# Kernel optimization log

Hardware: AMD Instinct MI355X
Metric: run time of the kernel (lower is better)

## Reference

```python
import jax, jax.numpy as jnp
import numpy as np

B, L, D = 4, 1024, 1024
H = 16
DH = D // H  # 64
CACHE_LEN = 1024


def setup_inputs() -> dict:
    key = jax.random.key(0)
    ks = jax.random.split(key, 12)
    s = 1.0 / np.sqrt(D)
    return {
        "query": jax.random.normal(ks[0], (B, L, D), jnp.float32),
        "key": jax.random.normal(ks[1], (B, L, D), jnp.float32),
        "value": jax.random.normal(ks[2], (B, L, D), jnp.float32),
        "cache": jax.random.normal(ks[3], (B, H, CACHE_LEN, 2 * DH), jnp.float32),
        "Wq": jax.random.normal(ks[4], (D, D), jnp.float32) * s,
        "bq": jnp.zeros((D,), jnp.float32),
        "Wk": jax.random.normal(ks[5], (D, D), jnp.float32) * s,
        "bk": jnp.zeros((D,), jnp.float32),
        "Wv": jax.random.normal(ks[6], (D, D), jnp.float32) * s,
        "bv": jnp.zeros((D,), jnp.float32),
        "Wo": jax.random.normal(ks[7], (D, D), jnp.float32) * s,
        "bo": jnp.zeros((D,), jnp.float32),
    }


def _split_heads(x):
    # (B, L, D) -> (B, H, L, DH)
    b, l, _ = x.shape
    return x.reshape(b, l, H, DH).transpose(0, 2, 1, 3)


def reference(query, key, value, cache, Wq, bq, Wk, bk, Wv, bv, Wo, bo):
    q = _split_heads(query @ Wq.T + bq)   # (B,H,Lq,DH)
    k = _split_heads(key @ Wk.T + bk)     # (B,H,Lk,DH)
    v = _split_heads(value @ Wv.T + bv)   # (B,H,Lk,DH)

    # KV-cache concat along sequence dim
    key_cache, value_cache = jnp.split(cache, 2, axis=-1)
    k = jnp.concatenate([key_cache, k], axis=2)   # (B,H,Lc+Lk,DH)
    v = jnp.concatenate([value_cache, v], axis=2)
    new_cache = jnp.concatenate([k, v], axis=-1)  # (B,H,Lc+Lk,2*DH)

    scores = jnp.einsum("bhqd,bhkd->bhqk", q, k) / jnp.sqrt(jnp.float32(DH))
    attn = jax.nn.softmax(scores, axis=-1)        # unmasked path (mask sentinel empty)
    out = jnp.einsum("bhqk,bhkd->bhqd", attn, v)  # (B,H,Lq,DH)
    out = out.transpose(0, 2, 1, 3).reshape(query.shape[0], -1, H * DH)
    out = out @ Wo.T + bo                         # (B,Lq,D)
    return (out, new_cache)
```

## Files before the change

kernel.cpp:

```cpp
#include <hip/hip_runtime.h>
#include <hip/hip_bf16.h>
#include <stdint.h>

constexpr int Hh = 16, Ll = 1024, Dd = 1024, DHh = 64, CL = 1024, TKV = 2048;
constexpr size_t OUT_ELEMS = 4ull * 1024 * 1024;
constexpr float LOG2E = 1.44269504088896340736f;

typedef __attribute__((ext_vector_type(8))) short short8;
typedef __attribute__((ext_vector_type(4))) float floatx4;

#define MFMA16(a, b, c) __builtin_amdgcn_mfma_f32_16x16x32_bf16(a, b, c, 0, 0, 0)

__device__ __forceinline__ float fexp2(float x) {
#if __has_builtin(__builtin_amdgcn_exp2f)
    return __builtin_amdgcn_exp2f(x);
#else
    float r;
    asm("v_exp_f32 %0, %1" : "=v"(r) : "v"(x));
    return r;
#endif
}

__device__ __forceinline__ short bfs(float x) {
    union { __hip_bfloat16 h; short s; } u;
    u.h = __float2bfloat16(x);
    return u.s;
}

__device__ __forceinline__ short8 cvt8(const float* p) {
    float4 a = *(const float4*)p;
    float4 b = *(const float4*)(p + 4);
    short8 r;
    r[0] = bfs(a.x); r[1] = bfs(a.y); r[2] = bfs(a.z); r[3] = bfs(a.w);
    r[4] = bfs(b.x); r[5] = bfs(b.y); r[6] = bfs(b.z); r[7] = bfs(b.w);
    return r;
}

__device__ __forceinline__ void gload_lds16(const __hip_bfloat16* g, __hip_bfloat16* l) {
    __builtin_amdgcn_global_load_lds((const __attribute__((address_space(1))) void*)g,
                                     (__attribute__((address_space(3))) void*)l, 16, 0, 0);
}

__device__ __forceinline__ int vswz(int d) { return ((d >> 3) ^ d) & 7; }

__global__ __launch_bounds__(256) void prep_kernel(
    const float* __restrict__ cache, const float* __restrict__ Wq,
    const float* __restrict__ Wk, const float* __restrict__ Wv,
    const float* __restrict__ Wo, float* __restrict__ outc,
    __hip_bfloat16* __restrict__ Wb, __hip_bfloat16* __restrict__ kbf,
    __hip_bfloat16* __restrict__ vbf) {
    if (blockIdx.x < 4096) {
        int c = blockIdx.x * 256 + threadIdx.x;
        int bh  = c >> 14;
        int rem = c & 16383;
        int t = rem >> 4, part = rem & 15;
        const float* s = cache + (size_t)c * 8;
        float* d = outc + OUT_ELEMS + (size_t)bh * 262144 + (size_t)rem * 8;
        *(float4*)d       = *(const float4*)s;
        *(float4*)(d + 4) = *(const float4*)(s + 4);
        short8 bv = cvt8(s);
        if (part < 8) {
            *(short8*)&kbf[(size_t)bh * 131072 + (size_t)t * 64 +
                           ((part ^ (t & 7)) << 3)] = bv;
        } else {
            int d0 = (part - 8) * 8;
#pragma unroll
            for (int e = 0; e < 8; e++) {
                int dd = d0 + e;
                ((short*)vbf)[((size_t)(bh * 16 + (t >> 7)) * 64 + dd) * 128 +
                              ((t & 127) ^ (vswz(dd) << 3))] = bv[e];
            }
        }
    } else {
        int c = (blockIdx.x - 4096) * 256 + threadIdx.x;
        int wsel = c >> 17;
        int within = c & 131071;
        const float* src = (wsel == 0) ? Wq : (wsel == 1) ? Wk : (wsel == 2) ? Wv : Wo;
        *(short8*)(Wb + (size_t)c * 8) = cvt8(src + (size_t)within * 8);
    }
}

__global__ __launch_bounds__(256) void gemm_qkv(
    const float* __restrict__ Aq, const float* __restrict__ Ak,
    const float* __restrict__ Av, const __hip_bfloat16* __restrict__ Wb,
    const float* __restrict__ bq, const float* __restrict__ bk,
    const float* __restrict__ bv, __hip_bfloat16* __restrict__ qws,
    float* __restrict__ outc, __hip_bfloat16* __restrict__ kbf,
    __hip_bfloat16* __restrict__ vbf) {
    constexpr int K = 1024, BK = 64;
    __shared__ alignas(16) __hip_bfloat16 As[64 * BK];
    __shared__ alignas(16) __hip_bfloat16 Bs[128 * BK];

    const int mode = blockIdx.z;
    const float* A = (mode == 0) ? Aq : (mode == 1) ? Ak : Av;
    const float* bias = (mode == 0) ? bq : (mode == 1) ? bk : bv;
    const __hip_bfloat16* W = Wb + ((size_t)mode << 20);

    const int tid = threadIdx.x;
    const int w = tid >> 6, lane = tid & 63;
    const int g = lane >> 4, lr = lane & 15;
    const int tm = blockIdx.x * 64, tn = blockIdx.y * 128;
    const int wr = (w >> 1) * 32, wc = (w & 1) * 64;

    floatx4 acc[2][4] = {};

    for (int k0 = 0; k0 < K; k0 += BK) {
        __syncthreads();
#pragma unroll
        for (int it = 0; it < 4; it++) {
            int c0 = it * 256 + w * 64;
            int c = c0 + lane;
            int row = c >> 3, col = (c & 7) * 8;
            gload_lds16(W + (size_t)(tn + row) * K + k0 + col, &Bs[c0 * 8]);
        }
#pragma unroll
        for (int it = 0; it < 2; it++) {
            int c = it * 256 + tid;
            int row = c >> 3, col = (c & 7) * 8;
            *(short8*)&As[c * 8] = cvt8(A + (size_t)(tm + row) * K + k0 + col);
        }
        __syncthreads();
#pragma unroll
        for (int kk = 0; kk < 2; kk++) {
            short8 af[2], bf[4];
#pragma unroll
            for (int i = 0; i < 2; i++)
                af[i] = *(const short8*)&As[(wr + i * 16 + lr) * BK + kk * 32 + g * 8];
#pragma unroll
            for (int j = 0; j < 4; j++)
                bf[j] = *(const short8*)&Bs[(wc + j * 16 + lr) * BK + kk * 32 + g * 8];
#pragma unroll
            for (int i = 0; i < 2; i++)
#pragma unroll
                for (int j = 0; j < 4; j++)
                    acc[i][j] = MFMA16(af[i], bf[j], acc[i][j]);
        }
    }

#pragma unroll
    for (int j = 0; j < 4; j++) {
        int n = tn + wc + j * 16 + lr;
        float bv_ = bias[n];
#pragma unroll
        for (int i = 0; i < 2; i++) {
#pragma unroll
            for (int r = 0; r < 4; r++) {
                int m = tm + wr + i * 16 + g * 4 + r;
                float v = acc[i][j][r] + bv_;
                if (mode == 0) {
                    size_t addr = (size_t)(m >> 10) * ((size_t)Hh * Ll * DHh) +
                                  (size_t)(n >> 6) * ((size_t)Ll * DHh) +
                                  (size_t)(m & 1023) * DHh + (n & 63);
                    qws[addr] = __float2bfloat16(v * (0.125f * LOG2E));
                } else {
                    size_t bh = (size_t)((m >> 10) * Hh + (n >> 6));
                    size_t addr = OUT_ELEMS + (bh * TKV + CL + (m & 1023)) * 128 + (n & 63) +
                                  (mode == 2 ? 64 : 0);
                    outc[addr] = v;
                    int t = CL + (m & 1023);
                    int dd = n & 63;
                    __hip_bfloat16 hv = __float2bfloat16(v);
                    if (mode == 1) {
                        kbf[bh * 131072 + (size_t)t * 64 +
                            (((dd >> 3) ^ (t & 7)) << 3) + (dd & 7)] = hv;
                    } else {
                        vbf[(bh * 16 + (size_t)(t >> 7)) * 8192 + (size_t)dd * 128 +
                            ((t & 127) ^ (vswz(dd) << 3))] = hv;
                    }
                }
            }
        }
    }
}

__global__ __launch_bounds__(256) void gemm_out(
    const __hip_bfloat16* __restrict__ A, const __hip_bfloat16* __restrict__ W,
    const float* __restrict__ bias, float* __restrict__ C) {
    constexpr int K = 1024, BK = 64;
    __shared__ alignas(16) __hip_bfloat16 As[64 * BK];
    __shared__ alignas(16) __hip_bfloat16 Bs[128 * BK];

    const int tid = threadIdx.x;
    const int w = tid >> 6, lane = tid & 63;
    const int g = lane >> 4, lr = lane & 15;
    const int tm = blockIdx.x * 64, tn = blockIdx.y * 128;
    const int wr = (w >> 1) * 32, wc = (w & 1) * 64;

    floatx4 acc[2][4] = {};

    for (int k0 = 0; k0 < K; k0 += BK) {
        __syncthreads();
#pragma unroll
        for (int it = 0; it < 4; it++) {
            int c0 = it * 256 + w * 64;
            int c = c0 + lane;
            int row = c >> 3, col = (c & 7) * 8;
            gload_lds16(W + (size_t)(tn + row) * K + k0 + col, &Bs[c0 * 8]);
        }
#pragma unroll
        for (int it = 0; it < 2; it++) {
            int c0 = it * 256 + w * 64;
            int c = c0 + lane;
            int row = c >> 3, col = (c & 7) * 8;
            gload_lds16(A + (size_t)(tm + row) * K + k0 + col, &As[c0 * 8]);
        }
        __syncthreads();
#pragma unroll
        for (int kk = 0; kk < 2; kk++) {
            short8 af[2], bf[4];
#pragma unroll
            for (int i = 0; i < 2; i++)
                af[i] = *(const short8*)&As[(wr + i * 16 + lr) * BK + kk * 32 + g * 8];
#pragma unroll
            for (int j = 0; j < 4; j++)
                bf[j] = *(const short8*)&Bs[(wc + j * 16 + lr) * BK + kk * 32 + g * 8];
#pragma unroll
            for (int i = 0; i < 2; i++)
#pragma unroll
                for (int j = 0; j < 4; j++)
                    acc[i][j] = MFMA16(af[i], bf[j], acc[i][j]);
        }
    }

#pragma unroll
    for (int j = 0; j < 4; j++) {
        int n = tn + wc + j * 16 + lr;
        float bv = bias[n];
#pragma unroll
        for (int i = 0; i < 2; i++)
#pragma unroll
            for (int r = 0; r < 4; r++) {
                int m = tm + wr + i * 16 + g * 4 + r;
                C[(size_t)m * 1024 + n] = acc[i][j][r] + bv;
            }
    }
}

__global__ __launch_bounds__(512) void attn_kernel(
    const __hip_bfloat16* __restrict__ qws, const __hip_bfloat16* __restrict__ kbf,
    const __hip_bfloat16* __restrict__ vbf, __hip_bfloat16* __restrict__ ows) {
    constexpr int KVB = 128;
    __shared__ alignas(16) __hip_bfloat16 Ks[2][KVB * 64];
    __shared__ alignas(16) __hip_bfloat16 Vt[2][64 * KVB];
    __shared__ alignas(16) __hip_bfloat16 Ps[8][32 * 136];

    const int tid = threadIdx.x;
    const int w = tid >> 6, lane = tid & 63;
    const int g = lane >> 4, lr = lane & 15;
    const int bh = blockIdx.x;
    const int q0 = blockIdx.y * 256 + w * 32;

    const __hip_bfloat16* qbase = qws + (size_t)bh * Ll * DHh;
    const __hip_bfloat16* kb = kbf + (size_t)bh * 131072;
    const __hip_bfloat16* vb = vbf + (size_t)bh * 131072;

    short8 qf[2][2];
#pragma unroll
    for (int i = 0; i < 2; i++)
#pragma unroll
        for (int kk = 0; kk < 2; kk++)
            qf[i][kk] = *(const short8*)
                (qbase + (size_t)(q0 + i * 16 + lr) * DHh + kk * 32 + g * 8);

#define STAGE(b, tl)                                                          \
    {                                                                         \
        const __hip_bfloat16* kt = kb + (size_t)(tl) * 8192;                  \
        const __hip_bfloat16* vt = vb + (size_t)(tl) * 8192;                  \
        _Pragma("unroll")                                                     \
        for (int it = 0; it < 2; it++) {                                      \
            int c0 = it * 512 + w * 64;                                       \
            gload_lds16(kt + (size_t)(c0 + lane) * 8, &Ks[b][c0 * 8]);        \
            gload_lds16(vt + (size_t)(c0 + lane) * 8, &Vt[b][c0 * 8]);        \
        }                                                                     \
    }

    float rm[2][4], rl[2][4];
    floatx4 o[2][4] = {};
#pragma unroll
    for (int i = 0; i < 2; i++)
#pragma unroll
        for (int j = 0; j < 4; j++) { rm[i][j] = -3e38f; rl[i][j] = 0.f; }

    STAGE(0, 0);
    __syncthreads();

    int cur = 0;
    for (int tl = 0; tl < 16; ++tl) {
        if (tl < 15) STAGE(cur ^ 1, tl + 1);

        floatx4 s[2][8] = {};
#pragma unroll
        for (int f = 0; f < 8; f++) {
            int row = f * 16 + lr;
#pragma unroll
            for (int kk = 0; kk < 2; kk++) {
                short8 bfr = *(const short8*)
                    &Ks[cur][row * 64 + (((kk * 4 + g) ^ (row & 7)) << 3)];
                s[0][f] = MFMA16(qf[0][kk], bfr, s[0][f]);
                s[1][f] = MFMA16(qf[1][kk], bfr, s[1][f]);
            }
        }

        bool ok = true;
        float mt[2][4];
#pragma unroll
        for (int i = 0; i < 2; i++)
#pragma unroll
            for (int j = 0; j < 4; j++) {
                float mv = fmaxf(
                    fmaxf(fmaxf(s[i][0][j], s[i][1][j]), fmaxf(s[i][2][j], s[i][3][j])),
                    fmaxf(fmaxf(s[i][4][j], s[i][5][j]), fmaxf(s[i][6][j], s[i][7][j])));
                mv = fmaxf(mv, __shfl_xor(mv, 1));
                mv = fmaxf(mv, __shfl_xor(mv, 2));
                mv = fmaxf(mv, __shfl_xor(mv, 4));
                mv = fmaxf(mv, __shfl_xor(mv, 8));
                mt[i][j] = mv;
                ok = ok && (mv - rm[i][j] <= 8.f);
            }
        if (!__all(ok)) {
#pragma unroll
            for (int i = 0; i < 2; i++)
#pragma unroll
                for (int j = 0; j < 4; j++) {
                    float mn = fmaxf(rm[i][j], mt[i][j]);
                    float corr = fexp2(rm[i][j] - mn);
                    rm[i][j] = mn;
                    rl[i][j] *= corr;
#pragma unroll
                    for (int f2 = 0; f2 < 4; f2++) o[i][f2][j] = o[i][f2][j] * corr;
                }
        }
#pragma unroll
        for (int i = 0; i < 2; i++) {
            float rs[4] = {0.f, 0.f, 0.f, 0.f};
#pragma unroll
            for (int f = 0; f < 8; f++)
#pragma unroll
                for (int j = 0; j < 4; j++) {
                    float p = fexp2(s[i][f][j] - rm[i][j]);
                    s[i][f][j] = p;
                    rs[j] += p;
                }
#pragma unroll
            for (int j = 0; j < 4; j++) {
                rs[j] += __shfl_xor(rs[j], 1);
                rs[j] += __shfl_xor(rs[j], 2);
                rs[j] += __shfl_xor(rs[j], 4);
                rs[j] += __shfl_xor(rs[j], 8);
                rl[i][j] += rs[j];
            }
        }

        __hip_bfloat16* pw = &Ps[w][0];
#pragma unroll
        for (int i = 0; i < 2; i++)
#pragma unroll
            for (int f = 0; f < 8; f++)
#pragma unroll
                for (int j = 0; j < 4; j++)
                    pw[(i * 16 + g * 4 + j) * 136 + f * 16 + lr] =
                        __float2bfloat16(s[i][f][j]);

#pragma unroll
        for (int kk = 0; kk < 4; kk++) {
            short8 pa0 = *(const short8*)&pw[(0 + lr) * 136 + kk * 32 + g * 8];
            short8 pa1 = *(const short8*)&pw[(16 + lr) * 136 + kk * 32 + g * 8];
#pragma unroll
            for (int f2 = 0; f2 < 4; f2++) {
                int d = f2 * 16 + lr;
                short8 vbr = *(const short8*)
                    &Vt[cur][d * KVB + ((kk * 32 + g * 8) ^ (vswz(d) << 3))];
                o[0][f2] = MFMA16(pa0, vbr, o[0][f2]);
                o[1][f2] = MFMA16(pa1, vbr, o[1][f2]);
            }
        }

        __syncthreads();
        cur ^= 1;
    }
#undef STAGE

    const int b = bh >> 4, h = bh & 15;
#pragma unroll
    for (int i = 0; i < 2; i++)
#pragma unroll
        for (int j = 0; j < 4; j++) {
            float inv = 1.0f / rl[i][j];
            int qrow = q0 + i * 16 + g * 4 + j;
            size_t rb = ((size_t)b * Ll + qrow) * Dd + (size_t)h * DHh;
#pragma unroll
            for (int f2 = 0; f2 < 4; f2++)
                ows[rb + f2 * 16 + lr] = __float2bfloat16(o[i][f2][j] * inv);
        }
}

extern "C" void kernel_launch(void* const* d_in, const int* in_sizes, int n_in,
                              void* d_out, int out_size, void* d_ws, size_t ws_size,
                              hipStream_t stream) {
    (void)in_sizes; (void)n_in; (void)out_size; (void)ws_size;
    const float* query = (const float*)d_in[0];
    const float* key   = (const float*)d_in[1];
    const float* value = (const float*)d_in[2];
    const float* cache = (const float*)d_in[3];
    const float* Wq = (const float*)d_in[4];
    const float* bq = (const float*)d_in[5];
    const float* Wk = (const float*)d_in[6];
    const float* bk = (const float*)d_in[7];
    const float* Wv = (const float*)d_in[8];
    const float* bv = (const float*)d_in[9];
    const float* Wo = (const float*)d_in[10];
    const float* bo = (const float*)d_in[11];

    float* out = (float*)d_out;
    __hip_bfloat16* qws = (__hip_bfloat16*)d_ws;
    __hip_bfloat16* aws = qws + OUT_ELEMS;
    __hip_bfloat16* Wb  = aws + OUT_ELEMS;
    __hip_bfloat16* kbf = Wb  + OUT_ELEMS;
    __hip_bfloat16* vbf = kbf + (8ull << 20);

    dim3 bb(256);
    prep_kernel<<<dim3(6144), bb, 0, stream>>>(cache, Wq, Wk, Wv, Wo, out, Wb, kbf, vbf);

    gemm_qkv<<<dim3(64, 8, 3), bb, 0, stream>>>(query, key, value, Wb, bq, bk, bv,
                                                qws, out, kbf, vbf);

    attn_kernel<<<dim3(64, 4), dim3(512), 0, stream>>>(qws, kbf, vbf, aws);

    gemm_out<<<dim3(64, 8), bb, 0, stream>>>(aws, Wb + (3u << 20), bo, out);
}
```

Before: 176.7 us.

## Move KV-cache copy and conversion into QKV GEMM launch as extra z-slice

The cache copy and bf16 conversion into the new_cache output and the K/V attention buffers now run in a fourth z-slice of the QKV GEMM grid. Each of those 512 blocks handles 2048 chunks. The standalone prep kernel is reduced to weight conversion only. This lets the memory-bound cache copy overlap with the compute-bound projection GEMM and shrinks the serial prep launch, but it puts bandwidth-heavy blocks alongside the GEMM blocks.

```diff
diff --git a/kernel.cpp b/kernel.cpp
--- a/kernel.cpp
+++ b/kernel.cpp
@@ -43,46 +43,21 @@
 
 __device__ __forceinline__ int vswz(int d) { return ((d >> 3) ^ d) & 7; }
 
-__global__ __launch_bounds__(256) void prep_kernel(
-    const float* __restrict__ cache, const float* __restrict__ Wq,
-    const float* __restrict__ Wk, const float* __restrict__ Wv,
-    const float* __restrict__ Wo, float* __restrict__ outc,
-    __hip_bfloat16* __restrict__ Wb, __hip_bfloat16* __restrict__ kbf,
-    __hip_bfloat16* __restrict__ vbf) {
-    if (blockIdx.x < 4096) {
-        int c = blockIdx.x * 256 + threadIdx.x;
-        int bh  = c >> 14;
-        int rem = c & 16383;
-        int t = rem >> 4, part = rem & 15;
-        const float* s = cache + (size_t)c * 8;
-        float* d = outc + OUT_ELEMS + (size_t)bh * 262144 + (size_t)rem * 8;
-        *(float4*)d       = *(const float4*)s;
-        *(float4*)(d + 4) = *(const float4*)(s + 4);
-        short8 bv = cvt8(s);
-        if (part < 8) {
-            *(short8*)&kbf[(size_t)bh * 131072 + (size_t)t * 64 +
-                           ((part ^ (t & 7)) << 3)] = bv;
-        } else {
-            int d0 = (part - 8) * 8;
-#pragma unroll
-            for (int e = 0; e < 8; e++) {
-                int dd = d0 + e;
-                ((short*)vbf)[((size_t)(bh * 16 + (t >> 7)) * 64 + dd) * 128 +
-                              ((t & 127) ^ (vswz(dd) << 3))] = bv[e];
-            }
-        }
-    } else {
-        int c = (blockIdx.x - 4096) * 256 + threadIdx.x;
-        int wsel = c >> 17;
-        int within = c & 131071;
-        const float* src = (wsel == 0) ? Wq : (wsel == 1) ? Wk : (wsel == 2) ? Wv : Wo;
-        *(short8*)(Wb + (size_t)c * 8) = cvt8(src + (size_t)within * 8);
-    }
+__global__ __launch_bounds__(256) void convert_w_kernel(
+    const float* __restrict__ Wq, const float* __restrict__ Wk,
+    const float* __restrict__ Wv, const float* __restrict__ Wo,
+    __hip_bfloat16* __restrict__ Wb) {
+    int c = blockIdx.x * 256 + threadIdx.x;
+    int wsel = c >> 17;
+    int within = c & 131071;
+    const float* src = (wsel == 0) ? Wq : (wsel == 1) ? Wk : (wsel == 2) ? Wv : Wo;
+    *(short8*)(Wb + (size_t)c * 8) = cvt8(src + (size_t)within * 8);
 }
 
 __global__ __launch_bounds__(256) void gemm_qkv(
     const float* __restrict__ Aq, const float* __restrict__ Ak,
-    const float* __restrict__ Av, const __hip_bfloat16* __restrict__ Wb,
+    const float* __restrict__ Av, const float* __restrict__ cache,
+    const __hip_bfloat16* __restrict__ Wb,
     const float* __restrict__ bq, const float* __restrict__ bk,
     const float* __restrict__ bv, __hip_bfloat16* __restrict__ qws,
     float* __restrict__ outc, __hip_bfloat16* __restrict__ kbf,
@@ -92,6 +67,35 @@
     __shared__ alignas(16) __hip_bfloat16 Bs[128 * BK];
 
     const int mode = blockIdx.z;
+    if (mode == 3) {
+        int id = blockIdx.y * 64 + blockIdx.x;
+#pragma unroll
+        for (int it = 0; it < 8; it++) {
+            int c = id * 2048 + it * 256 + threadIdx.x;
+            int bh  = c >> 14;
+            int rem = c & 16383;
+            int t = rem >> 4, part = rem & 15;
+            const float* s = cache + (size_t)c * 8;
+            float* d = outc + OUT_ELEMS + (size_t)bh * 262144 + (size_t)rem * 8;
+            *(float4*)d       = *(const float4*)s;
+            *(float4*)(d + 4) = *(const float4*)(s + 4);
+            short8 bv8 = cvt8(s);
+            if (part < 8) {
+                *(short8*)&kbf[(size_t)bh * 131072 + (size_t)t * 64 +
+                               ((part ^ (t & 7)) << 3)] = bv8;
+            } else {
+                int d0 = (part - 8) * 8;
+#pragma unroll
+                for (int e = 0; e < 8; e++) {
+                    int dd = d0 + e;
+                    ((short*)vbf)[((size_t)(bh * 16 + (t >> 7)) * 64 + dd) * 128 +
+                                  ((t & 127) ^ (vswz(dd) << 3))] = bv8[e];
+                }
+            }
+        }
+        return;
+    }
+
     const float* A = (mode == 0) ? Aq : (mode == 1) ? Ak : Av;
     const float* bias = (mode == 0) ? bq : (mode == 1) ? bk : bv;
     const __hip_bfloat16* W = Wb + ((size_t)mode << 20);
@@ -419,10 +423,10 @@
     __hip_bfloat16* vbf = kbf + (8ull << 20);
 
     dim3 bb(256);
-    prep_kernel<<<dim3(6144), bb, 0, stream>>>(cache, Wq, Wk, Wv, Wo, out, Wb, kbf, vbf);
-
-    gemm_qkv<<<dim3(64, 8, 3), bb, 0, stream>>>(query, key, value, Wb, bq, bk, bv,
-                                                qws, out, kbf, vbf);
+    convert_w_kernel<<<dim3(2048), bb, 0, stream>>>(Wq, Wk, Wv, Wo, Wb);
+
+    gemm_qkv<<<dim3(64, 8, 4), bb, 0, stream>>>(query, key, value, cache, Wb,
+                                                bq, bk, bv, qws, out, kbf, vbf);
 
     attn_kernel<<<dim3(64, 4), dim3(512), 0, stream>>>(qws, kbf, vbf, aws);
 
```

Result: no change. 175.0 us (-0.9%).
